# Optimization experiments

Hardware: AMD Instinct MI355X
Metric: run time of the kernel (lower is better)

Reference implementation:

```python
import jax, jax.numpy as jnp
import numpy as np

B, S, D, H = 2, 2048, 1024, 16
DK = D // H  # 64
EPS = 1e-5


def setup_inputs() -> dict:
    key = jax.random.key(0)
    ks = jax.random.split(key, 12)
    sc = 1.0 / np.sqrt(D)
    inp = {
        "Q": jax.random.normal(ks[0], (B, S, D), jnp.float32),
        "K": jax.random.normal(ks[1], (B, S, D), jnp.float32),
        "V": jax.random.normal(ks[2], (B, S, D), jnp.float32),
        # causal mask: True = masked out
        "attn_mask": jnp.broadcast_to(jnp.triu(jnp.ones((S, S), bool), k=1), (B, S, S)),
        # torch Linear weights stored [out, in]
        "Wq": jax.random.normal(ks[3], (D, D), jnp.float32) * sc,
        "bq": jnp.zeros((D,), jnp.float32),
        "Wk": jax.random.normal(ks[4], (D, D), jnp.float32) * sc,
        "bk": jnp.zeros((D,), jnp.float32),
        "Wv": jax.random.normal(ks[5], (D, D), jnp.float32) * sc,
        "bv": jnp.zeros((D,), jnp.float32),
        "Wo": jax.random.normal(ks[6], (D, D), jnp.float32) * sc,
        "bo": jnp.zeros((D,), jnp.float32),
        "gamma": jnp.ones((D,), jnp.float32),
        "beta": jnp.zeros((D,), jnp.float32),
    }
    return inp


def _layer_norm(x, gamma, beta):
    mu = jnp.mean(x, axis=-1, keepdims=True)
    var = jnp.mean(jnp.square(x - mu), axis=-1, keepdims=True)
    return (x - mu) * jax.lax.rsqrt(var + EPS) * gamma + beta


def reference(Q, K, V, attn_mask, Wq, bq, Wk, bk, Wv, bv, Wo, bo, gamma, beta):
    residual = Q
    # projections -> [B, H, S, DK]
    q = (Q @ Wq.T + bq).reshape(B, S, H, DK).transpose(0, 2, 1, 3)
    k = (K @ Wk.T + bk).reshape(B, S, H, DK).transpose(0, 2, 1, 3)
    v = (V @ Wv.T + bv).reshape(B, S, H, DK).transpose(0, 2, 1, 3)
    scores = jnp.einsum("bhqd,bhkd->bhqk", q, k) / np.sqrt(DK)
    scores = jnp.where(attn_mask[:, None, :, :], -1e9, scores)
    attn = jax.nn.softmax(scores, axis=-1)
    ctx = jnp.einsum("bhqk,bhkd->bhqd", attn, v)  # [B,H,S,DK]
    ctx = ctx.transpose(0, 2, 1, 3).reshape(B, S, H * DK)
    out = ctx @ Wo.T + bo
    return _layer_norm(out + residual, gamma, beta), attn
```

## Files before the change

### kernel.cpp

```cpp
#include <hip/hip_runtime.h>
#include <hip/hip_fp16.h>

#define BB 2
#define SS 2048
#define DD 1024
#define HH 16
#define DKK 64
#define BHH (BB*HH)
#define MM (BB*SS)
#define EPSF 1e-5f

typedef _Float16 f16;
typedef _Float16 f16x4 __attribute__((ext_vector_type(4)));
typedef _Float16 f16x8 __attribute__((ext_vector_type(8)));
typedef float f32x4 __attribute__((ext_vector_type(4)));

__device__ __forceinline__ int swz128(int row, int byteInRow) {
    return row * 128 + (byteInRow ^ ((row & 7) << 4));
}

__device__ __forceinline__ void gl_lds16(const f16* g, f16* l) {
    __builtin_amdgcn_global_load_lds((const __attribute__((address_space(1))) void*)g,
                                     (__attribute__((address_space(3))) void*)l, 16, 0, 0);
}

__global__ __launch_bounds__(256) void cvt_pass(
    const float* __restrict__ s0, const float* __restrict__ s1, const float* __restrict__ s2,
    const float* __restrict__ s3, const float* __restrict__ s4, const float* __restrict__ s5,
    const float* __restrict__ s6,
    f16* __restrict__ d0, f16* __restrict__ d1, f16* __restrict__ d2,
    f16* __restrict__ d3, f16* __restrict__ d4, f16* __restrict__ d5, f16* __restrict__ d6)
{
    const int y = blockIdx.y;
    const float* s; f16* d; int n4;
    switch (y) {
        case 0: s = s0; d = d0; n4 = (MM * DD) / 4; break;
        case 1: s = s1; d = d1; n4 = (MM * DD) / 4; break;
        case 2: s = s2; d = d2; n4 = (MM * DD) / 4; break;
        case 3: s = s3; d = d3; n4 = (DD * DD) / 4; break;
        case 4: s = s4; d = d4; n4 = (DD * DD) / 4; break;
        case 5: s = s5; d = d5; n4 = (DD * DD) / 4; break;
        default: s = s6; d = d6; n4 = (DD * DD) / 4; break;
    }
    for (int i = blockIdx.x * 256 + threadIdx.x; i < n4; i += 256 * 256) {
        f32x4 v = ((const f32x4*)s)[i];
        f16x4 h = { (f16)v.x, (f16)v.y, (f16)v.z, (f16)v.w };
        ((f16x4*)d)[i] = h;
    }
}

__global__ __launch_bounds__(256) void qkv_gemm(
    const f16* __restrict__ Qf, const f16* __restrict__ Kf, const f16* __restrict__ Vf,
    const f16* __restrict__ Wqf, const float* __restrict__ bq,
    const f16* __restrict__ Wkf, const float* __restrict__ bk,
    const f16* __restrict__ Wvf, const float* __restrict__ bv,
    f16* __restrict__ qh, f16* __restrict__ kh, f16* __restrict__ vTh)
{
    const int type = blockIdx.z;
    const f16* X = (type == 0) ? Qf : (type == 1) ? Kf : Vf;
    const f16* W = (type == 0) ? Wqf : (type == 1) ? Wkf : Wvf;
    const float* bias = (type == 0) ? bq : (type == 1) ? bk : bv;
    const int m0 = blockIdx.y * 128, n0 = blockIdx.x * 128;

    __shared__ f16 smem[2][128 * 64];
    f16* a_lds = smem[0];
    f16* b_lds = smem[1];

    const int t = threadIdx.x;
    const int l = t & 63, w = t >> 6;
    const int wr = (w >> 1) * 64, wc = (w & 1) * 64;

    f32x4 acc[4][4] = {};

    for (int k0 = 0; k0 < DD; k0 += 64) {
        __syncthreads();
        #pragma unroll
        for (int p = 0; p < 4; p++) {
            int idx = w * 4 + p;
            int gci = idx * 64 + l;
            int row = gci >> 3, slot = gci & 7;
            int ss = slot ^ (row & 7);
            gl_lds16(X + (size_t)(m0 + row) * DD + k0 + ss * 8, a_lds + idx * 512);
            gl_lds16(W + (size_t)(n0 + row) * DD + k0 + ss * 8, b_lds + idx * 512);
        }
        __syncthreads();
        #pragma unroll
        for (int kk = 0; kk < 2; kk++) {
            f16x8 af[4], bf[4];
            #pragma unroll
            for (int mi = 0; mi < 4; mi++) {
                int row = wr + mi * 16 + (l & 15);
                af[mi] = *(const f16x8*)((const char*)a_lds + swz128(row, kk * 64 + (l >> 4) * 16));
            }
            #pragma unroll
            for (int ni = 0; ni < 4; ni++) {
                int row = wc + ni * 16 + (l & 15);
                bf[ni] = *(const f16x8*)((const char*)b_lds + swz128(row, kk * 64 + (l >> 4) * 16));
            }
            #pragma unroll
            for (int mi = 0; mi < 4; mi++)
                #pragma unroll
                for (int ni = 0; ni < 4; ni++)
                    acc[mi][ni] = __builtin_amdgcn_mfma_f32_16x16x32_f16(af[mi], bf[ni], acc[mi][ni], 0, 0, 0);
        }
    }

    if (type == 2) {
        __syncthreads();
        f16* tb = smem[0];
        #pragma unroll
        for (int mi = 0; mi < 4; mi++) {
            #pragma unroll
            for (int ni = 0; ni < 4; ni++) {
                int nl = wc + ni * 16 + (l & 15);
                int mb = (wr + mi * 16 + (l >> 4) * 4) * 2;
                f16x4 hv;
                #pragma unroll
                for (int r = 0; r < 4; r++)
                    hv[r] = (f16)(acc[mi][ni][r] + bias[n0 + nl]);
                *(f16x4*)((char*)tb + nl * 256 + (mb ^ ((nl & 7) << 4))) = hv;
            }
        }
        __syncthreads();
        const int b = m0 >> 11;
        const int mloc = m0 & (SS - 1);
        #pragma unroll
        for (int i = 0; i < 8; i++) {
            int o = w * 8192 + i * 1024 + l * 16;
            int nl = o >> 8;
            int inb = o & 255;
            f16x8 v = *(const f16x8*)((char*)tb + nl * 256 + (inb ^ ((nl & 7) << 4)));
            int ng = n0 + nl, h_ = ng >> 6, dk = ng & 63;
            int s = mloc + inb / 2;
            *(f16x8*)(vTh + ((size_t)((b * HH + h_) * DKK + dk)) * SS + s) = v;
        }
    } else {
        #pragma unroll
        for (int mi = 0; mi < 4; mi++) {
            #pragma unroll
            for (int ni = 0; ni < 4; ni++) {
                #pragma unroll
                for (int r = 0; r < 4; r++) {
                    int m = m0 + wr + mi * 16 + (l >> 4) * 4 + r;
                    int n = n0 + wc + ni * 16 + (l & 15);
                    float v = acc[mi][ni][r] + bias[n];
                    f16 hv = (f16)v;
                    int b = m >> 11, s = m & (SS - 1);
                    int h_ = n >> 6, dk = n & (DKK - 1);
                    f16* dst = (type == 0) ? qh : kh;
                    dst[((size_t)((b * HH + h_) * SS + s)) * DKK + dk] = hv;
                }
            }
        }
    }
}

__global__ __launch_bounds__(256) void attn_kernel(
    const f16* __restrict__ qh, const f16* __restrict__ kh, const f16* __restrict__ vTh,
    float* __restrict__ attn_out, f16* __restrict__ ctx)
{
    const int bid = blockIdx.x;
    const int swz = (bid & 7) * 128 + (bid >> 3);
    const int bh = swz >> 5;
    const int qb = 31 - (swz & 31);
    const int qbase = qb * 64;
    const int t = threadIdx.x, l = t & 63, w = t >> 6;
    const int c = l & 15, g = l >> 4;

    __shared__ f16 kb3[3][64 * 64];
    __shared__ f16 vb3[3][64 * 64];

    const float CSC = 0.125f * 1.44269504f;
    const int nj = qb + 1;
    const int qloc = w * 16 + c;
    const int qglob = qbase + qloc;

    const f16* kbase = kh + (size_t)bh * SS * DKK;
    const f16* vbase = vTh + (size_t)bh * DKK * SS;
    float* aout = attn_out + (size_t)bh * SS * SS;

    const f16* qsrc = qh + (size_t)bh * SS * DKK + (size_t)qglob * DKK;
    f16x8 bq[2];
    bq[0] = *(const f16x8*)(qsrc + g * 8);
    bq[1] = *(const f16x8*)(qsrc + 32 + g * 8);

    #define STAGE_K(jt, buf) { \
        const f16* ksrc_ = kbase + (size_t)(jt) * 64 * DKK; \
        _Pragma("unroll") \
        for (int p = 0; p < 2; p++) { \
            int idx = w * 2 + p; \
            int gci = idx * 64 + l; \
            int row = gci >> 3, slot = gci & 7; \
            int ss_ = slot ^ (row & 7); \
            gl_lds16(ksrc_ + row * DKK + ss_ * 8, kb3[buf] + idx * 512); \
        } }
    #define STAGE_V(jt, buf) { \
        const f16* vsrc_ = vbase + (size_t)(jt) * 64; \
        _Pragma("unroll") \
        for (int p = 0; p < 2; p++) { \
            int idx = w * 2 + p; \
            int gci = idx * 64 + l; \
            int row = gci >> 3, slot = gci & 7; \
            int ss_ = slot ^ (row & 7); \
            gl_lds16(vsrc_ + (size_t)row * SS + ss_ * 8, vb3[buf] + idx * 512); \
        } }

    #define QKT(dstf, srcb) { \
        __builtin_amdgcn_s_setprio(1); \
        _Pragma("unroll") \
        for (int dw = 0; dw < 2; dw++) { \
            _Pragma("unroll") \
            for (int ni = 0; ni < 4; ni++) { \
                f16x8 ak = *(const f16x8*)((const char*)(srcb) + swz128(ni * 16 + c, dw * 64 + g * 16)); \
                dstf[ni] = __builtin_amdgcn_mfma_f32_16x16x32_f16(ak, bq[dw], dstf[ni], 0, 0, 0); \
            } \
        } \
        __builtin_amdgcn_s_setprio(0); }

    #define PSTORE(jt) { \
        float* pl_ = (float*)vb3; \
        _Pragma("unroll") \
        for (int i = 0; i < 4; i++) { \
            int row_ = w * 16 + 4 * i + g; \
            f32x4 v_ = *(const f32x4*)((char*)pl_ + row_ * 256 + ((c * 16) ^ ((row_ & 7) << 4))); \
            __builtin_nontemporal_store(v_, (f32x4*)(aout + (size_t)(qbase + row_) * SS + (jt) * 64 + c * 4)); \
        } }

    #define CBAR(n) { asm volatile("s_waitcnt vmcnt(" #n ")"); \
                      __builtin_amdgcn_s_barrier(); \
                      __builtin_amdgcn_sched_barrier(0); }

    STAGE_K(0, 0);
    if (nj > 1) STAGE_K(1, 1);
    STAGE_V(0, 0);
    CBAR(0);

    float lrow = 0.f;
    f32x4 cacc[4] = {};
    f32x4 sprev[4];

    for (int j = 0; j < nj; j++) {
        if (j + 2 < nj) STAGE_K(j + 2, (j + 2) % 3);
        if (j + 1 < nj) STAGE_V(j + 1, (j + 1) % 3);

        f32x4 scur[4] = {};
        QKT(scur, kb3[j % 3]);

        if (j > 0) {
            const f16* pvv = vb3[(j - 1) % 3];
            f16x4 bfr[4];
            #pragma unroll
            for (int ni = 0; ni < 4; ni++) {
                float e0 = exp2f(sprev[ni][0] * CSC);
                float e1 = exp2f(sprev[ni][1] * CSC);
                float e2 = exp2f(sprev[ni][2] * CSC);
                float e3 = exp2f(sprev[ni][3] * CSC);
                lrow += e0 + e1 + e2 + e3;
                bfr[ni] = f16x4{ (f16)e0, (f16)e1, (f16)e2, (f16)e3 };
            }
            __builtin_amdgcn_s_setprio(1);
            #pragma unroll
            for (int ni2 = 0; ni2 < 4; ni2++) {
                #pragma unroll
                for (int nk = 0; nk < 4; nk++) {
                    f16x4 av = *(const f16x4*)((const char*)pvv + swz128(ni2 * 16 + c, nk * 32 + g * 8));
                    cacc[ni2] = __builtin_amdgcn_mfma_f32_16x16x16f16(av, bfr[nk], cacc[ni2], 0, 0, 0);
                }
            }
            __builtin_amdgcn_s_setprio(0);
        }

        if (j + 3 <= nj)      CBAR(4)
        else if (j + 2 == nj) CBAR(2)
        else                  CBAR(0);

        #pragma unroll
        for (int x = 0; x < 4; x++) sprev[x] = scur[x];
    }

    STAGE_K(0, 0);
    if (nj > 1) STAGE_K(1, 1);

    {
        const f16* pvv = vb3[(nj - 1) % 3];
        f16x4 bfr[4];
        #pragma unroll
        for (int ni = 0; ni < 4; ni++) {
            int kkb = ni * 16 + 4 * g;
            float e0 = (kkb + 0 > qloc) ? 0.f : exp2f(sprev[ni][0] * CSC);
            float e1 = (kkb + 1 > qloc) ? 0.f : exp2f(sprev[ni][1] * CSC);
            float e2 = (kkb + 2 > qloc) ? 0.f : exp2f(sprev[ni][2] * CSC);
            float e3 = (kkb + 3 > qloc) ? 0.f : exp2f(sprev[ni][3] * CSC);
            lrow += e0 + e1 + e2 + e3;
            bfr[ni] = f16x4{ (f16)e0, (f16)e1, (f16)e2, (f16)e3 };
        }
        __builtin_amdgcn_s_setprio(1);
        #pragma unroll
        for (int ni2 = 0; ni2 < 4; ni2++) {
            #pragma unroll
            for (int nk = 0; nk < 4; nk++) {
                f16x4 av = *(const f16x4*)((const char*)pvv + swz128(ni2 * 16 + c, nk * 32 + g * 8));
                cacc[ni2] = __builtin_amdgcn_mfma_f32_16x16x16f16(av, bfr[nk], cacc[ni2], 0, 0, 0);
            }
        }
        __builtin_amdgcn_s_setprio(0);
    }

    lrow += __shfl_xor(lrow, 16);
    lrow += __shfl_xor(lrow, 32);
    const float rinv = 1.f / lrow;
    const float nls = -__log2f(lrow);

    {
        int b = bh >> 4, h_ = bh & 15;
        f16* cbase = ctx + (size_t)(b * SS + qglob) * DD + h_ * 64;
        #pragma unroll
        for (int ni2 = 0; ni2 < 4; ni2++) {
            f16x4 hv = { (f16)(cacc[ni2][0] * rinv), (f16)(cacc[ni2][1] * rinv),
                         (f16)(cacc[ni2][2] * rinv), (f16)(cacc[ni2][3] * rinv) };
            *(f16x4*)(cbase + ni2 * 16 + 4 * g) = hv;
        }
    }

    CBAR(0);

    {
        float* pl = (float*)vb3;
        for (int j = 0; j < nj; j++) {
            if (j + 2 < nj) STAGE_K(j + 2, (j + 2) % 3);

            f32x4 scur[4] = {};
            QKT(scur, kb3[j % 3]);

            if (j > 0) {
                #pragma unroll
                for (int ni = 0; ni < 4; ni++) {
                    f32x4 st = { exp2f(fmaf(sprev[ni][0], CSC, nls)),
                                 exp2f(fmaf(sprev[ni][1], CSC, nls)),
                                 exp2f(fmaf(sprev[ni][2], CSC, nls)),
                                 exp2f(fmaf(sprev[ni][3], CSC, nls)) };
                    *(f32x4*)((char*)pl + (w * 16 + c) * 256 + ((ni * 64 + g * 16) ^ ((c & 7) << 4))) = st;
                }
                PSTORE(j - 1);
            }

            if (j == 0 && j + 2 < nj)  CBAR(2)
            else if (j + 2 < nj)       CBAR(6)
            else if (j > 0)            CBAR(4)
            else                       CBAR(0);

            #pragma unroll
            for (int x = 0; x < 4; x++) sprev[x] = scur[x];
        }

        {
            #pragma unroll
            for (int ni = 0; ni < 4; ni++) {
                int kkb = ni * 16 + 4 * g;
                f32x4 st = { (kkb + 0 > qloc) ? 0.f : exp2f(fmaf(sprev[ni][0], CSC, nls)),
                             (kkb + 1 > qloc) ? 0.f : exp2f(fmaf(sprev[ni][1], CSC, nls)),
                             (kkb + 2 > qloc) ? 0.f : exp2f(fmaf(sprev[ni][2], CSC, nls)),
                             (kkb + 3 > qloc) ? 0.f : exp2f(fmaf(sprev[ni][3], CSC, nls)) };
                *(f32x4*)((char*)pl + (w * 16 + c) * 256 + ((ni * 64 + g * 16) ^ ((c & 7) << 4))) = st;
            }
            PSTORE(nj - 1);
        }
    }

    {
        f32x4 z = { 0.f, 0.f, 0.f, 0.f };
        for (int jb = qb + 1; jb < 32; jb++) {
            #pragma unroll
            for (int i = 0; i < 4; i++) {
                int c2 = t + 256 * i;
                int row = c2 >> 4, cg = c2 & 15;
                __builtin_nontemporal_store(z, (f32x4*)(aout + (size_t)(qbase + row) * SS + jb * 64 + cg * 4));
            }
        }
    }
    #undef STAGE_K
    #undef STAGE_V
    #undef QKT
    #undef PSTORE
    #undef CBAR
}

__global__ __launch_bounds__(256) void oproj_gemm(
    const f16* __restrict__ A, const f16* __restrict__ Wof, const float* __restrict__ bo,
    const float* __restrict__ resid, float* __restrict__ out)
{
    const int m0 = blockIdx.y * 128, n0 = blockIdx.x * 128;
    __shared__ f16 a_lds[128 * 64];
    __shared__ f16 b_lds[128 * 64];
    const int t = threadIdx.x;
    const int l = t & 63, w = t >> 6;
    const int wr = (w >> 1) * 64, wc = (w & 1) * 64;

    f32x4 acc[4][4] = {};

    for (int k0 = 0; k0 < DD; k0 += 64) {
        __syncthreads();
        #pragma unroll
        for (int p = 0; p < 4; p++) {
            int idx = w * 4 + p;
            int gci = idx * 64 + l;
            int row = gci >> 3, slot = gci & 7;
            int ss = slot ^ (row & 7);
            gl_lds16(A + (size_t)(m0 + row) * DD + k0 + ss * 8, a_lds + idx * 512);
            gl_lds16(Wof + (size_t)(n0 + row) * DD + k0 + ss * 8, b_lds + idx * 512);
        }
        __syncthreads();
        #pragma unroll
        for (int kk = 0; kk < 2; kk++) {
            f16x8 af[4], bf[4];
            #pragma unroll
            for (int mi = 0; mi < 4; mi++) {
                int row = wr + mi * 16 + (l & 15);
                af[mi] = *(const f16x8*)((const char*)a_lds + swz128(row, kk * 64 + (l >> 4) * 16));
            }
            #pragma unroll
            for (int ni = 0; ni < 4; ni++) {
                int row = wc + ni * 16 + (l & 15);
                bf[ni] = *(const f16x8*)((const char*)b_lds + swz128(row, kk * 64 + (l >> 4) * 16));
            }
            #pragma unroll
            for (int mi = 0; mi < 4; mi++)
                #pragma unroll
                for (int ni = 0; ni < 4; ni++)
                    acc[mi][ni] = __builtin_amdgcn_mfma_f32_16x16x32_f16(af[mi], bf[ni], acc[mi][ni], 0, 0, 0);
        }
    }

    #pragma unroll
    for (int mi = 0; mi < 4; mi++) {
        #pragma unroll
        for (int ni = 0; ni < 4; ni++) {
            #pragma unroll
            for (int r = 0; r < 4; r++) {
                int m = m0 + wr + mi * 16 + (l >> 4) * 4 + r;
                int n = n0 + wc + ni * 16 + (l & 15);
                float v = acc[mi][ni][r] + bo[n] + resid[(size_t)m * DD + n];
                out[(size_t)m * DD + n] = v;
            }
        }
    }
}

__global__ __launch_bounds__(256) void ln_kernel(
    const float* __restrict__ x, const float* __restrict__ gamma,
    const float* __restrict__ beta, float* __restrict__ out)
{
    int row = blockIdx.x;
    int t = threadIdx.x;
    float4 v = ((const float4*)(x + (size_t)row * DD))[t];
    float s = v.x + v.y + v.z + v.w;
    __shared__ float red[4];
    #pragma unroll
    for (int o = 32; o; o >>= 1) s += __shfl_down(s, o, 64);
    if ((t & 63) == 0) red[t >> 6] = s;
    __syncthreads();
    float mean = (red[0] + red[1] + red[2] + red[3]) * (1.f / DD);
    __syncthreads();
    float4 d;
    d.x = v.x - mean; d.y = v.y - mean; d.z = v.z - mean; d.w = v.w - mean;
    float q = d.x * d.x + d.y * d.y + d.z * d.z + d.w * d.w;
    #pragma unroll
    for (int o = 32; o; o >>= 1) q += __shfl_down(q, o, 64);
    if ((t & 63) == 0) red[t >> 6] = q;
    __syncthreads();
    float var = (red[0] + red[1] + red[2] + red[3]) * (1.f / DD);
    float rstd = rsqrtf(var + EPSF);
    float4 g = ((const float4*)gamma)[t];
    float4 bt = ((const float4*)beta)[t];
    float4 o4;
    o4.x = d.x * rstd * g.x + bt.x;
    o4.y = d.y * rstd * g.y + bt.y;
    o4.z = d.z * rstd * g.z + bt.z;
    o4.w = d.w * rstd * g.w + bt.w;
    ((float4*)(out + (size_t)row * DD))[t] = o4;
}

extern "C" void kernel_launch(void* const* d_in, const int* in_sizes, int n_in,
                              void* d_out, int out_size, void* d_ws, size_t ws_size,
                              hipStream_t stream)
{
    const float* Q     = (const float*)d_in[0];
    const float* K     = (const float*)d_in[1];
    const float* V     = (const float*)d_in[2];
    const float* Wq    = (const float*)d_in[4];
    const float* bq    = (const float*)d_in[5];
    const float* Wk    = (const float*)d_in[6];
    const float* bk    = (const float*)d_in[7];
    const float* Wv    = (const float*)d_in[8];
    const float* bv    = (const float*)d_in[9];
    const float* Wo    = (const float*)d_in[10];
    const float* bo    = (const float*)d_in[11];
    const float* gamma = (const float*)d_in[12];
    const float* beta  = (const float*)d_in[13];

    float* out_ln   = (float*)d_out;
    float* attn_out = (float*)d_out + (size_t)BB * SS * DD;

    f16* Qf  = (f16*)attn_out;
    f16* Kf  = Qf + (size_t)MM * DD;
    f16* Vf  = Kf + (size_t)MM * DD;
    f16* Wqf = (f16*)out_ln;
    f16* Wkf = Wqf + (size_t)DD * DD;
    f16* Wvf = Wkf + (size_t)DD * DD;
    f16* Wof = Wvf + (size_t)DD * DD;

    char* ws = (char*)d_ws;
    f16*   qh    = (f16*)(ws);
    f16*   kh    = (f16*)(ws + ((size_t)8  << 20));
    f16*   vTh   = (f16*)(ws + ((size_t)16 << 20));
    f16*   ctx   = (f16*)(ws + ((size_t)24 << 20));
    float* oproj = (float*)(ws + ((size_t)32 << 20));

    cvt_pass<<<dim3(256, 7), 256, 0, stream>>>(Q, K, V, Wq, Wk, Wv, Wo,
                                               Qf, Kf, Vf, Wqf, Wkf, Wvf, Wof);
    qkv_gemm<<<dim3(8, 32, 3), 256, 0, stream>>>(Qf, Kf, Vf, Wqf, bq, Wkf, bk, Wvf, bv, qh, kh, vTh);
    attn_kernel<<<dim3(1024), 256, 0, stream>>>(qh, kh, vTh, attn_out, ctx);
    oproj_gemm<<<dim3(8, 32), 256, 0, stream>>>(ctx, Wof, bo, Q, oproj);
    ln_kernel<<<dim3(MM), 256, 0, stream>>>(oproj, gamma, beta, out_ln);
}
```

Baseline: 219.8 us.

## Double-buffer LDS tiles in QKV and output projection GEMMs

```diff
diff --git a/kernel.cpp b/kernel.cpp
--- a/kernel.cpp
+++ b/kernel.cpp
@@ -62,9 +62,8 @@
     const float* bias = (type == 0) ? bq : (type == 1) ? bk : bv;
     const int m0 = blockIdx.y * 128, n0 = blockIdx.x * 128;
 
-    __shared__ f16 smem[2][128 * 64];
-    f16* a_lds = smem[0];
-    f16* b_lds = smem[1];
+    __shared__ f16 a_lds[2][128 * 64];
+    __shared__ f16 b_lds[2][128 * 64];
 
     const int t = threadIdx.x;
     const int l = t & 63, w = t >> 6;
@@ -72,42 +71,52 @@
 
     f32x4 acc[4][4] = {};
 
-    for (int k0 = 0; k0 < DD; k0 += 64) {
-        __syncthreads();
-        #pragma unroll
-        for (int p = 0; p < 4; p++) {
-            int idx = w * 4 + p;
-            int gci = idx * 64 + l;
-            int row = gci >> 3, slot = gci & 7;
-            int ss = slot ^ (row & 7);
-            gl_lds16(X + (size_t)(m0 + row) * DD + k0 + ss * 8, a_lds + idx * 512);
-            gl_lds16(W + (size_t)(n0 + row) * DD + k0 + ss * 8, b_lds + idx * 512);
-        }
-        __syncthreads();
+    #define QKV_STAGE(kt, buf) { \
+        _Pragma("unroll") \
+        for (int p = 0; p < 4; p++) { \
+            int idx = w * 4 + p; \
+            int gci = idx * 64 + l; \
+            int row = gci >> 3, slot = gci & 7; \
+            int ss = slot ^ (row & 7); \
+            gl_lds16(X + (size_t)(m0 + row) * DD + (kt) * 64 + ss * 8, a_lds[buf] + idx * 512); \
+            gl_lds16(W + (size_t)(n0 + row) * DD + (kt) * 64 + ss * 8, b_lds[buf] + idx * 512); \
+        } }
+
+    QKV_STAGE(0, 0);
+    for (int k0 = 0; k0 < 16; k0++) {
+        asm volatile("s_waitcnt vmcnt(0)");
+        __builtin_amdgcn_s_barrier();
+        __builtin_amdgcn_sched_barrier(0);
+        if (k0 + 1 < 16) QKV_STAGE(k0 + 1, (k0 + 1) & 1);
+        const f16* al = a_lds[k0 & 1];
+        const f16* bl = b_lds[k0 & 1];
         #pragma unroll
         for (int kk = 0; kk < 2; kk++) {
             f16x8 af[4], bf[4];
             #pragma unroll
             for (int mi = 0; mi < 4; mi++) {
                 int row = wr + mi * 16 + (l & 15);
-                af[mi] = *(const f16x8*)((const char*)a_lds + swz128(row, kk * 64 + (l >> 4) * 16));
+                af[mi] = *(const f16x8*)((const char*)al + swz128(row, kk * 64 + (l >> 4) * 16));
             }
             #pragma unroll
             for (int ni = 0; ni < 4; ni++) {
                 int row = wc + ni * 16 + (l & 15);
-                bf[ni] = *(const f16x8*)((const char*)b_lds + swz128(row, kk * 64 + (l >> 4) * 16));
-            }
+                bf[ni] = *(const f16x8*)((const char*)bl + swz128(row, kk * 64 + (l >> 4) * 16));
+            }
+            __builtin_amdgcn_s_setprio(1);
             #pragma unroll
             for (int mi = 0; mi < 4; mi++)
                 #pragma unroll
                 for (int ni = 0; ni < 4; ni++)
                     acc[mi][ni] = __builtin_amdgcn_mfma_f32_16x16x32_f16(af[mi], bf[ni], acc[mi][ni], 0, 0, 0);
-        }
-    }
+            __builtin_amdgcn_s_setprio(0);
+        }
+    }
+    #undef QKV_STAGE
 
     if (type == 2) {
         __syncthreads();
-        f16* tb = smem[0];
+        f16* tb = (f16*)a_lds;
         #pragma unroll
         for (int mi = 0; mi < 4; mi++) {
             #pragma unroll
@@ -390,46 +399,56 @@
     const float* __restrict__ resid, float* __restrict__ out)
 {
     const int m0 = blockIdx.y * 128, n0 = blockIdx.x * 128;
-    __shared__ f16 a_lds[128 * 64];
-    __shared__ f16 b_lds[128 * 64];
+    __shared__ f16 a_lds[2][128 * 64];
+    __shared__ f16 b_lds[2][128 * 64];
     const int t = threadIdx.x;
     const int l = t & 63, w = t >> 6;
     const int wr = (w >> 1) * 64, wc = (w & 1) * 64;
 
     f32x4 acc[4][4] = {};
 
-    for (int k0 = 0; k0 < DD; k0 += 64) {
-        __syncthreads();
-        #pragma unroll
-        for (int p = 0; p < 4; p++) {
-            int idx = w * 4 + p;
-            int gci = idx * 64 + l;
-            int row = gci >> 3, slot = gci & 7;
-            int ss = slot ^ (row & 7);
-            gl_lds16(A + (size_t)(m0 + row) * DD + k0 + ss * 8, a_lds + idx * 512);
-            gl_lds16(Wof + (size_t)(n0 + row) * DD + k0 + ss * 8, b_lds + idx * 512);
-        }
-        __syncthreads();
+    #define OP_STAGE(kt, buf) { \
+        _Pragma("unroll") \
+        for (int p = 0; p < 4; p++) { \
+            int idx = w * 4 + p; \
+            int gci = idx * 64 + l; \
+            int row = gci >> 3, slot = gci & 7; \
+            int ss = slot ^ (row & 7); \
+            gl_lds16(A + (size_t)(m0 + row) * DD + (kt) * 64 + ss * 8, a_lds[buf] + idx * 512); \
+            gl_lds16(Wof + (size_t)(n0 + row) * DD + (kt) * 64 + ss * 8, b_lds[buf] + idx * 512); \
+        } }
+
+    OP_STAGE(0, 0);
+    for (int k0 = 0; k0 < 16; k0++) {
+        asm volatile("s_waitcnt vmcnt(0)");
+        __builtin_amdgcn_s_barrier();
+        __builtin_amdgcn_sched_barrier(0);
+        if (k0 + 1 < 16) OP_STAGE(k0 + 1, (k0 + 1) & 1);
+        const f16* al = a_lds[k0 & 1];
+        const f16* bl = b_lds[k0 & 1];
         #pragma unroll
         for (int kk = 0; kk < 2; kk++) {
             f16x8 af[4], bf[4];
             #pragma unroll
             for (int mi = 0; mi < 4; mi++) {
                 int row = wr + mi * 16 + (l & 15);
-                af[mi] = *(const f16x8*)((const char*)a_lds + swz128(row, kk * 64 + (l >> 4) * 16));
+                af[mi] = *(const f16x8*)((const char*)al + swz128(row, kk * 64 + (l >> 4) * 16));
             }
             #pragma unroll
             for (int ni = 0; ni < 4; ni++) {
                 int row = wc + ni * 16 + (l & 15);
-                bf[ni] = *(const f16x8*)((const char*)b_lds + swz128(row, kk * 64 + (l >> 4) * 16));
-            }
+                bf[ni] = *(const f16x8*)((const char*)bl + swz128(row, kk * 64 + (l >> 4) * 16));
+            }
+            __builtin_amdgcn_s_setprio(1);
             #pragma unroll
             for (int mi = 0; mi < 4; mi++)
                 #pragma unroll
                 for (int ni = 0; ni < 4; ni++)
                     acc[mi][ni] = __builtin_amdgcn_mfma_f32_16x16x32_f16(af[mi], bf[ni], acc[mi][ni], 0, 0, 0);
-        }
-    }
+            __builtin_amdgcn_s_setprio(0);
+        }
+    }
+    #undef OP_STAGE
 
     #pragma unroll
     for (int mi = 0; mi < 4; mi++) {
```

After: 213.2 us. -3.0%, faster.
